# Kernel optimization log

Measured on AMD Instinct MI355X. Metric: run time of the kernel, lower is better.

## Reference

```python
import jax, jax.numpy as jnp
import numpy as np

HIDDEN = 256
RELD = 2
CAT = HIDDEN * 5 + 3  # 1283
LN_EPS = 1e-5


def setup_inputs() -> dict:
    key = jax.random.key(0)
    ks = jax.random.split(key, 13)
    b, m, h, d = 4, 256, 64, HIDDEN
    inp = {
        "point_token": jax.random.normal(ks[0], (b, m, d), jnp.float32),
        "step_hidden": jax.random.normal(ks[1], (b, h, d), jnp.float32),
        "point_dyn": jax.random.normal(ks[2], (b, m, h, d), jnp.float32),
        "point_sem": jax.random.normal(ks[3], (b, m, h, d), jnp.float32),
        "point_identity_trace": jax.random.normal(ks[4], (b, m, h, d), jnp.float32),
        "rel_pred": jax.random.normal(ks[5], (b, m, h, RELD), jnp.float32),
        "vis_prob": jax.random.uniform(ks[6], (b, m, h), jnp.float32),
        # learned params (torch Linear init scale ~ 1/sqrt(fan_in))
        "ln_gamma": jnp.ones((CAT,), jnp.float32),
        "ln_beta": jnp.zeros((CAT,), jnp.float32),
        "W1": jax.random.normal(ks[7], (CAT, d), jnp.float32) / np.sqrt(CAT),  # stored (in, out)
        "b1": jax.random.normal(ks[8], (d,), jnp.float32) / np.sqrt(CAT),
        "W2": jax.random.normal(ks[9], (d, d), jnp.float32) / np.sqrt(d),
        "b2": jax.random.normal(ks[10], (d,), jnp.float32) / np.sqrt(d),
    }
    return inp


def _forward(point_token, step_hidden, point_dyn, point_sem, point_identity_trace,
             rel_pred, vis_prob, ln_gamma, ln_beta, W1, b1, W2, b2):
    b, m, h, _ = rel_pred.shape
    x = jnp.concatenate([
        jnp.broadcast_to(point_token[:, :, None, :], (b, m, h, point_token.shape[-1])),
        jnp.broadcast_to(step_hidden[:, None, :, :], (b, m, h, step_hidden.shape[-1])),
        point_dyn,
        point_sem,
        point_identity_trace,
        rel_pred,
        vis_prob[:, :, :, None],
    ], axis=-1)  # (b, m, h, 5*d+3)
    # LayerNorm over last dim
    mu = jnp.mean(x, axis=-1, keepdims=True)
    var = jnp.mean(jnp.square(x - mu), axis=-1, keepdims=True)
    x = (x - mu) * jax.lax.rsqrt(var + LN_EPS) * ln_gamma + ln_beta
    # Linear -> GELU -> Linear -> GELU (exact erf GELU as in torch default)
    y = jax.nn.gelu(jnp.einsum('bmhc,cd->bmhd', x, W1) + b1, approximate=False)
    y = jax.nn.gelu(jnp.einsum('bmhd,de->bmhe', y, W2) + b2, approximate=False)
    return y


def reference(point_token, step_hidden, point_dyn, point_sem, point_identity_trace,
              rel_pred, vis_prob, ln_gamma, ln_beta, W1, b1, W2, b2):
    return _forward(point_token, step_hidden, point_dyn, point_sem,
                    point_identity_trace, rel_pred, vis_prob,
                    ln_gamma, ln_beta, W1, b1, W2, b2)
```

## Files before the change

### kernel.cpp

```cpp
#include <hip/hip_runtime.h>


typedef float  f32x4 __attribute__((ext_vector_type(4)));
typedef short  s16x8 __attribute__((ext_vector_type(8)));

__device__ __forceinline__ unsigned short f2bf(float f) {
    unsigned u = __builtin_bit_cast(unsigned, f);
    return (unsigned short)((u + 0x7fffu + ((u >> 16) & 1u)) >> 16);
}
__device__ __forceinline__ unsigned f2bf_pk(float lo, float hi) {
    unsigned ulo = __builtin_bit_cast(unsigned, lo);
    unsigned uhi = __builtin_bit_cast(unsigned, hi);
    ulo = (ulo + 0x7fffu + ((ulo >> 16) & 1u)) >> 16;
    uhi = (uhi + 0x7fffu + ((uhi >> 16) & 1u)) & 0xffff0000u;
    return ulo | uhi;
}
__device__ __forceinline__ float gelu_t(float x) {
    float u2 = 1.5957691216057308f * x + 0.07135481627f * (x * x * x);
    float e  = __expf(u2);
    float r  = __builtin_amdgcn_rcpf(e + 1.0f);
    return x - x * r;
}

__global__ void __launch_bounds__(256)
prep_k(const float* __restrict__ W1, const float* __restrict__ W2,
       const float* __restrict__ gamma, const float* __restrict__ beta,
       float* __restrict__ Sg, float* __restrict__ Sb,
       short* __restrict__ w1t, short* __restrict__ w2t)
{
    __shared__ float tile[32][257];
    const int blk = blockIdx.x;
    const int t   = threadIdx.x;
    const int nl  = t >> 2, c = t & 3;
    if (blk < 40) {
        float sg = 0.f, sb = 0.f;
#pragma unroll 4
        for (int kl = 0; kl < 32; ++kl) {
            int k = blk * 32 + kl;
            float w  = W1[k * 256 + t];
            float gv = gamma[k];
            tile[kl][t] = gv * w;
            sg += gv * w;
            sb += beta[k] * w;
        }
        atomicAdd(&Sg[t], sg);
        atomicAdd(&Sb[t], sb);
        __syncthreads();
#pragma unroll
        for (int gi = 0; gi < 4; ++gi) {
            int n = gi * 64 + nl;
            uint4 o;
            o.x = f2bf_pk(tile[c*8+0][n], tile[c*8+1][n]);
            o.y = f2bf_pk(tile[c*8+2][n], tile[c*8+3][n]);
            o.z = f2bf_pk(tile[c*8+4][n], tile[c*8+5][n]);
            o.w = f2bf_pk(tile[c*8+6][n], tile[c*8+7][n]);
            *(uint4*)(w1t + (blk * 256 + n) * 32 + c * 8) = o;
        }
    } else {
        const int kb = blk - 40;
#pragma unroll 4
        for (int kl = 0; kl < 32; ++kl) {
            int k = kb * 32 + kl;
            tile[kl][t] = W2[k * 256 + t];
        }
        __syncthreads();
#pragma unroll
        for (int gi = 0; gi < 4; ++gi) {
            int n = gi * 64 + nl;
            uint4 o;
            o.x = f2bf_pk(tile[c*8+0][n], tile[c*8+1][n]);
            o.y = f2bf_pk(tile[c*8+2][n], tile[c*8+3][n]);
            o.z = f2bf_pk(tile[c*8+4][n], tile[c*8+5][n]);
            o.w = f2bf_pk(tile[c*8+6][n], tile[c*8+7][n]);
            *(uint4*)(w2t + (kb * 256 + n) * 32 + c * 8) = o;
        }
    }
}

__global__ void __launch_bounds__(256, 2)
fused_main(const float* __restrict__ token, const float* __restrict__ step,
           const float* __restrict__ dyn,   const float* __restrict__ sem,
           const float* __restrict__ trace, const float* __restrict__ rel,
           const float* __restrict__ vis,   const float* __restrict__ gamma,
           const float* __restrict__ beta,  const float* __restrict__ W1,
           const float* __restrict__ b1v,   const float* __restrict__ b2v,
           const float* __restrict__ Sg,    const float* __restrict__ Sb,
           const short* __restrict__ w1t,   const short* __restrict__ w2t,
           float* __restrict__ out)
{
    __shared__ __align__(16) char lds_raw[66816];
    uint4* As                 = (uint4*)lds_raw;
    unsigned long long* As8   = (unsigned long long*)lds_raw;
    float* pst                = (float*)(lds_raw + 32768);
    float* y1f                = (float*)lds_raw;
    float* mu_s               = (float*)(lds_raw + 65536);
    float* rs_s               = mu_s + 64;
    float* t0s                = mu_s + 128;
    float* t1s                = mu_s + 192;
    float* t2s                = mu_s + 256;

    const int t    = threadIdx.x;
    const int bm   = blockIdx.x;
    const int b_i  = bm >> 8;
    const int lane = t & 63;
    const int wv   = t >> 6;
    const int l15  = lane & 15;
    const int q    = lane >> 4;
    const int n0   = wv * 64;
    const int r0   = wv * 16;

    const float* base0 = token + bm * 256;
    const float* base1 = step  + (b_i * 64 + r0) * 256;
    const float* base2 = dyn   + (bm * 64 + r0) * 256;
    const float* base3 = sem   + (bm * 64 + r0) * 256;
    const float* base4 = trace + (bm * 64 + r0) * 256;

    f32x4 acc[4][4];
    float s1[16], s2[16];
#pragma unroll
    for (int i = 0; i < 4; ++i)
#pragma unroll
        for (int j = 0; j < 4; ++j)
            acc[i][j] = (f32x4){0.f, 0.f, 0.f, 0.f};
#pragma unroll
    for (int j = 0; j < 16; ++j) { s1[j] = 0.f; s2[j] = 0.f; }

    float4 g[16];

#define LOAD_SEG(BASE, STRIDE)                                                 \
    _Pragma("unroll")                                                          \
    for (int j = 0; j < 16; ++j)                                               \
        g[j] = *((const float4*)((BASE) + j * (STRIDE)) + lane);

#define STATS_CVT_WRITE()                                                      \
    _Pragma("unroll")                                                          \
    for (int j = 0; j < 16; ++j) {                                             \
        float4 v = g[j];                                                       \
        s1[j] += v.x + v.y + v.z + v.w;                                        \
        s2[j] += v.x*v.x + v.y*v.y + v.z*v.z + v.w*v.w;                        \
        int m_ = r0 + j;                                                       \
        unsigned long long pk_ = (unsigned long long)f2bf_pk(v.x, v.y)         \
                               | ((unsigned long long)f2bf_pk(v.z, v.w) << 32);\
        As8[(m_ * 32 + ((lane >> 1) ^ (j & 7))) * 2 + (lane & 1)] = pk_;       \
    }

#define MFMA_SEG(SEG)                                                          \
    _Pragma("unroll")                                                          \
    for (int kc = 0; kc < 8; ++kc) {                                           \
        const short* wk_ = w1t + ((SEG) * 8 + kc) * 8192;                      \
        s16x8 bfr[4];                                                          \
        _Pragma("unroll")                                                      \
        for (int nt = 0; nt < 4; ++nt)                                         \
            bfr[nt] = *(const s16x8*)(wk_ + (n0 + nt * 16 + l15) * 32 + q * 8);\
        s16x8 afr[4];                                                          \
        _Pragma("unroll")                                                      \
        for (int mt = 0; mt < 4; ++mt) {                                       \
            int m_ = mt * 16 + l15;                                            \
            afr[mt] = *(const s16x8*)&As[m_ * 32 + ((kc * 4 + q) ^ (m_ & 7))]; \
        }                                                                      \
        _Pragma("unroll")                                                      \
        for (int mt = 0; mt < 4; ++mt)                                         \
            _Pragma("unroll")                                                  \
            for (int nt = 0; nt < 4; ++nt)                                     \
                acc[mt][nt] = __builtin_amdgcn_mfma_f32_16x16x32_bf16(         \
                    afr[mt], bfr[nt], acc[mt][nt], 0, 0, 0);                   \
    }

    LOAD_SEG(base0, 0);
    STATS_CVT_WRITE();
    __syncthreads();
    LOAD_SEG(base1, 256);
    MFMA_SEG(0);
    __syncthreads();
    STATS_CVT_WRITE();
    __syncthreads();
    LOAD_SEG(base2, 256);
    MFMA_SEG(1);
    __syncthreads();
    STATS_CVT_WRITE();
    __syncthreads();
    LOAD_SEG(base3, 256);
    MFMA_SEG(2);
    __syncthreads();
    STATS_CVT_WRITE();
    __syncthreads();
    LOAD_SEG(base4, 256);
    MFMA_SEG(3);
    __syncthreads();
    STATS_CVT_WRITE();
    __syncthreads();
    MFMA_SEG(4);

#pragma unroll
    for (int j = 0; j < 16; ++j) {
        int r  = r0 + j;
        int ci = (((lane >> 2) ^ (j & 7)) << 2) + (lane & 3);
        pst[r * 64 + ci]        = s1[j];
        pst[4096 + r * 64 + ci] = s2[j];
    }
    __syncthreads();

    if (t < 64) {
        const int r = t;
        float S1 = 0.f, S2 = 0.f;
#pragma unroll
        for (int i = 0; i < 16; ++i) {
            int c = i ^ (r & 7);
            const f32x4 a = *(const f32x4*)&pst[r * 64 + (c << 2)];
            const f32x4 b = *(const f32x4*)&pst[4096 + r * 64 + (c << 2)];
            S1 += a[0] + a[1] + a[2] + a[3];
            S2 += b[0] + b[1] + b[2] + b[3];
        }
        float x0 = rel[(bm * 64 + r) * 2 + 0];
        float x1 = rel[(bm * 64 + r) * 2 + 1];
        float x2 = vis[bm * 64 + r];
        S1 += x0 + x1 + x2;
        S2 += x0 * x0 + x1 * x1 + x2 * x2;
        const float inv = 1.0f / 1283.0f;
        float mu  = S1 * inv;
        float var = S2 * inv - mu * mu;
        float rs  = rsqrtf(var + 1e-5f);
        mu_s[r] = mu;
        rs_s[r] = rs;
        t0s[r] = (x0 - mu) * rs * gamma[1280] + beta[1280];
        t1s[r] = (x1 - mu) * rs * gamma[1281] + beta[1281];
        t2s[r] = (x2 - mu) * rs * gamma[1282] + beta[1282];
    }
    __syncthreads();

#pragma unroll
    for (int nt = 0; nt < 4; ++nt) {
        int n = n0 + nt * 16 + l15;
        float sg  = Sg[n], sb = Sb[n], bb = b1v[n];
        float wt0 = W1[1280 * 256 + n];
        float wt1 = W1[1281 * 256 + n];
        float wt2 = W1[1282 * 256 + n];
#pragma unroll
        for (int mt = 0; mt < 4; ++mt) {
#pragma unroll
            for (int r4 = 0; r4 < 4; ++r4) {
                int r = mt * 16 + q * 4 + r4;
                float rsv = rs_s[r], muv = mu_s[r];
                float v = rsv * acc[mt][nt][r4] - rsv * muv * sg + sb + bb
                        + t0s[r] * wt0 + t1s[r] * wt1 + t2s[r] * wt2;
                v = gelu_t(v);
                y1f[r * 256 + ((((n >> 2) ^ (r & 7)) << 2) | (n & 3))] = v;
            }
        }
    }
    __syncthreads();

    f32x4 acc2[4][4];
#pragma unroll
    for (int i = 0; i < 4; ++i)
#pragma unroll
        for (int j = 0; j < 4; ++j)
            acc2[i][j] = (f32x4){0.f, 0.f, 0.f, 0.f};

#pragma unroll
    for (int kc = 0; kc < 8; ++kc) {
        const short* wk = w2t + kc * 8192;
        s16x8 bfr[4];
#pragma unroll
        for (int nt = 0; nt < 4; ++nt)
            bfr[nt] = *(const s16x8*)(wk + (n0 + nt * 16 + l15) * 32 + q * 8);
        s16x8 afr[4];
#pragma unroll
        for (int mt = 0; mt < 4; ++mt) {
            int m  = mt * 16 + l15;
            int s  = m & 7;
            int c0 = kc * 8 + q * 2;
            const f32x4 lo = *(const f32x4*)&y1f[m * 256 + ((c0 ^ s) << 2)];
            const f32x4 hi = *(const f32x4*)&y1f[m * 256 + (((c0 + 1) ^ s) << 2)];
            unsigned p0, p1, p2, p3;
            asm("v_cvt_pk_bf16_f32 %0, %1, %2" : "=v"(p0) : "v"(lo[0]), "v"(lo[1]));
            asm("v_cvt_pk_bf16_f32 %0, %1, %2" : "=v"(p1) : "v"(lo[2]), "v"(lo[3]));
            asm("v_cvt_pk_bf16_f32 %0, %1, %2" : "=v"(p2) : "v"(hi[0]), "v"(hi[1]));
            asm("v_cvt_pk_bf16_f32 %0, %1, %2" : "=v"(p3) : "v"(hi[2]), "v"(hi[3]));
            uint4 u;
            u.x = p0; u.y = p1; u.z = p2; u.w = p3;
            afr[mt] = __builtin_bit_cast(s16x8, u);
        }
#pragma unroll
        for (int mt = 0; mt < 4; ++mt)
#pragma unroll
            for (int nt = 0; nt < 4; ++nt)
                acc2[mt][nt] = __builtin_amdgcn_mfma_f32_16x16x32_bf16(
                    afr[mt], bfr[nt], acc2[mt][nt], 0, 0, 0);
    }

#pragma unroll
    for (int nt = 0; nt < 4; ++nt) {
        int n = n0 + nt * 16 + l15;
        float bb = b2v[n];
#pragma unroll
        for (int mt = 0; mt < 4; ++mt)
#pragma unroll
            for (int r4 = 0; r4 < 4; ++r4) {
                int r = mt * 16 + q * 4 + r4;
                out[(bm * 64 + r) * 256 + n] = gelu_t(acc2[mt][nt][r4] + bb);
            }
    }
#undef LOAD_SEG
#undef STATS_CVT_WRITE
#undef MFMA_SEG
}

extern "C" void kernel_launch(void* const* d_in, const int* in_sizes, int n_in,
                              void* d_out, int out_size, void* d_ws, size_t ws_size,
                              hipStream_t stream) {
    const float* token = (const float*)d_in[0];
    const float* step  = (const float*)d_in[1];
    const float* dyn   = (const float*)d_in[2];
    const float* sem   = (const float*)d_in[3];
    const float* trace = (const float*)d_in[4];
    const float* rel   = (const float*)d_in[5];
    const float* vis   = (const float*)d_in[6];
    const float* gamma = (const float*)d_in[7];
    const float* beta  = (const float*)d_in[8];
    const float* W1    = (const float*)d_in[9];
    const float* b1    = (const float*)d_in[10];
    const float* W2    = (const float*)d_in[11];
    const float* b2    = (const float*)d_in[12];

    float* Sg  = (float*)d_ws;
    float* Sb  = Sg + 256;
    short* w1t = (short*)((char*)d_ws + 2048);
    short* w2t = w1t + 1280 * 256;
    float* out = (float*)d_out;

    hipMemsetAsync(d_ws, 0, 2048, stream);
    hipLaunchKernelGGL(prep_k, dim3(48), dim3(256), 0, stream,
                       W1, W2, gamma, beta, Sg, Sb, w1t, w2t);
    hipLaunchKernelGGL(fused_main, dim3(1024), dim3(256), 0, stream,
                       token, step, dyn, sem, trace, rel, vis, gamma, beta,
                       W1, b1, b2, Sg, Sb, w1t, w2t, out);
}
```

Baseline: 306.5 us.

## Double-buffer LDS segments with 8 waves and shuffle-based LayerNorm stats

The main kernel moves from 4 to 8 waves per block, each wave owning 8 rows for loading and 32 output columns for the GEMMs. It ping-pongs between two LDS buffers so the bf16 pack and global loads of the next segment overlap the MFMA work on the current one, and it raises MFMA issue priority with s_setprio. Row statistics are now reduced with wave shuffles instead of an LDS staging pass. The prep kernel computes the gamma/beta column sums in a dedicated block, which removes the memset and the atomics. In exchange, each wave does less MFMA work per A-fragment load, and launch_bounds(512,4) with about 66KB of LDS per block may not reach the occupancy it asks for.

```diff
diff --git a/kernel.cpp b/kernel.cpp
--- a/kernel.cpp
+++ b/kernel.cpp
@@ -33,18 +33,11 @@
     const int t   = threadIdx.x;
     const int nl  = t >> 2, c = t & 3;
     if (blk < 40) {
-        float sg = 0.f, sb = 0.f;
 #pragma unroll 4
         for (int kl = 0; kl < 32; ++kl) {
             int k = blk * 32 + kl;
-            float w  = W1[k * 256 + t];
-            float gv = gamma[k];
-            tile[kl][t] = gv * w;
-            sg += gv * w;
-            sb += beta[k] * w;
-        }
-        atomicAdd(&Sg[t], sg);
-        atomicAdd(&Sb[t], sb);
+            tile[kl][t] = gamma[k] * W1[k * 256 + t];
+        }
         __syncthreads();
 #pragma unroll
         for (int gi = 0; gi < 4; ++gi) {
@@ -56,7 +49,7 @@
             o.w = f2bf_pk(tile[c*8+6][n], tile[c*8+7][n]);
             *(uint4*)(w1t + (blk * 256 + n) * 32 + c * 8) = o;
         }
-    } else {
+    } else if (blk < 48) {
         const int kb = blk - 40;
 #pragma unroll 4
         for (int kl = 0; kl < 32; ++kl) {
@@ -74,10 +67,21 @@
             o.w = f2bf_pk(tile[c*8+6][n], tile[c*8+7][n]);
             *(uint4*)(w2t + (kb * 256 + n) * 32 + c * 8) = o;
         }
-    }
-}
-
-__global__ void __launch_bounds__(256, 2)
+    } else {
+        const int n = t;
+        float sg = 0.f, sb = 0.f;
+#pragma unroll 8
+        for (int k = 0; k < 1280; ++k) {
+            float w = W1[k * 256 + n];
+            sg += gamma[k] * w;
+            sb += beta[k]  * w;
+        }
+        Sg[n] = sg;
+        Sb[n] = sb;
+    }
+}
+
+__global__ void __launch_bounds__(512, 4)
 fused_main(const float* __restrict__ token, const float* __restrict__ step,
            const float* __restrict__ dyn,   const float* __restrict__ sem,
            const float* __restrict__ trace, const float* __restrict__ rel,
@@ -89,9 +93,10 @@
            float* __restrict__ out)
 {
     __shared__ __align__(16) char lds_raw[66816];
-    uint4* As                 = (uint4*)lds_raw;
-    unsigned long long* As8   = (unsigned long long*)lds_raw;
-    float* pst                = (float*)(lds_raw + 32768);
+    uint4* bufA               = (uint4*)lds_raw;
+    uint4* bufB               = (uint4*)(lds_raw + 32768);
+    unsigned long long* bufA8 = (unsigned long long*)lds_raw;
+    unsigned long long* bufB8 = (unsigned long long*)(lds_raw + 32768);
     float* y1f                = (float*)lds_raw;
     float* mu_s               = (float*)(lds_raw + 65536);
     float* rs_s               = mu_s + 64;
@@ -106,8 +111,9 @@
     const int wv   = t >> 6;
     const int l15  = lane & 15;
     const int q    = lane >> 4;
-    const int n0   = wv * 64;
-    const int r0   = wv * 16;
+    const int sw   = l15 & 7;
+    const int n0   = wv * 32;
+    const int r0   = wv * 8;
 
     const float* base0 = token + bm * 256;
     const float* base1 = step  + (b_i * 64 + r0) * 256;
@@ -115,121 +121,126 @@
     const float* base3 = sem   + (bm * 64 + r0) * 256;
     const float* base4 = trace + (bm * 64 + r0) * 256;
 
-    f32x4 acc[4][4];
-    float s1[16], s2[16];
+    f32x4 acc[2][2];
+    float s1[8], s2[8];
+    float4 g[8];
+    unsigned long long pk[8];
+#pragma unroll
+    for (int i = 0; i < 2; ++i)
+#pragma unroll
+        for (int j = 0; j < 2; ++j)
+            acc[i][j] = (f32x4){0.f, 0.f, 0.f, 0.f};
+    f32x4 acc4[4][2];
 #pragma unroll
     for (int i = 0; i < 4; ++i)
 #pragma unroll
-        for (int j = 0; j < 4; ++j)
-            acc[i][j] = (f32x4){0.f, 0.f, 0.f, 0.f};
-#pragma unroll
-    for (int j = 0; j < 16; ++j) { s1[j] = 0.f; s2[j] = 0.f; }
-
-    float4 g[16];
-
-#define LOAD_SEG(BASE, STRIDE)                                                 \
+        for (int j = 0; j < 2; ++j)
+            acc4[i][j] = (f32x4){0.f, 0.f, 0.f, 0.f};
+#pragma unroll
+    for (int j = 0; j < 8; ++j) { s1[j] = 0.f; s2[j] = 0.f; }
+
+#define LOADSEG(BASE, STRIDE)                                                  \
     _Pragma("unroll")                                                          \
-    for (int j = 0; j < 16; ++j)                                               \
+    for (int j = 0; j < 8; ++j)                                                \
         g[j] = *((const float4*)((BASE) + j * (STRIDE)) + lane);
 
-#define STATS_CVT_WRITE()                                                      \
+#define PACKSEG()                                                              \
     _Pragma("unroll")                                                          \
-    for (int j = 0; j < 16; ++j) {                                             \
+    for (int j = 0; j < 8; ++j) {                                              \
         float4 v = g[j];                                                       \
         s1[j] += v.x + v.y + v.z + v.w;                                        \
         s2[j] += v.x*v.x + v.y*v.y + v.z*v.z + v.w*v.w;                        \
-        int m_ = r0 + j;                                                       \
-        unsigned long long pk_ = (unsigned long long)f2bf_pk(v.x, v.y)         \
-                               | ((unsigned long long)f2bf_pk(v.z, v.w) << 32);\
-        As8[(m_ * 32 + ((lane >> 1) ^ (j & 7))) * 2 + (lane & 1)] = pk_;       \
-    }
-
-#define MFMA_SEG(SEG)                                                          \
+        pk[j] = (unsigned long long)f2bf_pk(v.x, v.y)                          \
+              | ((unsigned long long)f2bf_pk(v.z, v.w) << 32);                 \
+    }
+
+#define WRITESEG(BUF8)                                                         \
     _Pragma("unroll")                                                          \
-    for (int kc = 0; kc < 8; ++kc) {                                           \
-        const short* wk_ = w1t + ((SEG) * 8 + kc) * 8192;                      \
-        s16x8 bfr[4];                                                          \
-        _Pragma("unroll")                                                      \
-        for (int nt = 0; nt < 4; ++nt)                                         \
-            bfr[nt] = *(const s16x8*)(wk_ + (n0 + nt * 16 + l15) * 32 + q * 8);\
-        s16x8 afr[4];                                                          \
-        _Pragma("unroll")                                                      \
-        for (int mt = 0; mt < 4; ++mt) {                                       \
-            int m_ = mt * 16 + l15;                                            \
-            afr[mt] = *(const s16x8*)&As[m_ * 32 + ((kc * 4 + q) ^ (m_ & 7))]; \
-        }                                                                      \
-        _Pragma("unroll")                                                      \
-        for (int mt = 0; mt < 4; ++mt)                                         \
-            _Pragma("unroll")                                                  \
-            for (int nt = 0; nt < 4; ++nt)                                     \
-                acc[mt][nt] = __builtin_amdgcn_mfma_f32_16x16x32_bf16(         \
-                    afr[mt], bfr[nt], acc[mt][nt], 0, 0, 0);                   \
-    }
-
-    LOAD_SEG(base0, 0);
-    STATS_CVT_WRITE();
-    __syncthreads();
-    LOAD_SEG(base1, 256);
-    MFMA_SEG(0);
-    __syncthreads();
-    STATS_CVT_WRITE();
-    __syncthreads();
-    LOAD_SEG(base2, 256);
-    MFMA_SEG(1);
-    __syncthreads();
-    STATS_CVT_WRITE();
-    __syncthreads();
-    LOAD_SEG(base3, 256);
-    MFMA_SEG(2);
-    __syncthreads();
-    STATS_CVT_WRITE();
-    __syncthreads();
-    LOAD_SEG(base4, 256);
-    MFMA_SEG(3);
-    __syncthreads();
-    STATS_CVT_WRITE();
-    __syncthreads();
-    MFMA_SEG(4);
-
-#pragma unroll
-    for (int j = 0; j < 16; ++j) {
-        int r  = r0 + j;
-        int ci = (((lane >> 2) ^ (j & 7)) << 2) + (lane & 3);
-        pst[r * 64 + ci]        = s1[j];
-        pst[4096 + r * 64 + ci] = s2[j];
-    }
-    __syncthreads();
-
-    if (t < 64) {
-        const int r = t;
-        float S1 = 0.f, S2 = 0.f;
-#pragma unroll
-        for (int i = 0; i < 16; ++i) {
-            int c = i ^ (r & 7);
-            const f32x4 a = *(const f32x4*)&pst[r * 64 + (c << 2)];
-            const f32x4 b = *(const f32x4*)&pst[4096 + r * 64 + (c << 2)];
-            S1 += a[0] + a[1] + a[2] + a[3];
-            S2 += b[0] + b[1] + b[2] + b[3];
-        }
-        float x0 = rel[(bm * 64 + r) * 2 + 0];
-        float x1 = rel[(bm * 64 + r) * 2 + 1];
-        float x2 = vis[bm * 64 + r];
-        S1 += x0 + x1 + x2;
-        S2 += x0 * x0 + x1 * x1 + x2 * x2;
-        const float inv = 1.0f / 1283.0f;
-        float mu  = S1 * inv;
-        float var = S2 * inv - mu * mu;
-        float rs  = rsqrtf(var + 1e-5f);
-        mu_s[r] = mu;
-        rs_s[r] = rs;
-        t0s[r] = (x0 - mu) * rs * gamma[1280] + beta[1280];
-        t1s[r] = (x1 - mu) * rs * gamma[1281] + beta[1281];
-        t2s[r] = (x2 - mu) * rs * gamma[1282] + beta[1282];
-    }
-    __syncthreads();
-
-#pragma unroll
-    for (int nt = 0; nt < 4; ++nt) {
+    for (int j = 0; j < 8; ++j)                                                \
+        (BUF8)[((r0 + j) * 32 + ((lane >> 1) ^ j)) * 2 + (lane & 1)] = pk[j];
+
+#define G1_KC(SEG, KC, BUF)                                                    \
+    do {                                                                       \
+        const short* wk_ = w1t + ((SEG) * 8 + (KC)) * 8192;                    \
+        s16x8 b0 = *(const s16x8*)(wk_ + (n0 + l15) * 32 + q * 8);             \
+        s16x8 b1 = *(const s16x8*)(wk_ + (n0 + 16 + l15) * 32 + q * 8);        \
+        s16x8 a0 = *(const s16x8*)&(BUF)[( 0 + l15) * 32 + (((KC)*4+q) ^ sw)]; \
+        s16x8 a1 = *(const s16x8*)&(BUF)[(16 + l15) * 32 + (((KC)*4+q) ^ sw)]; \
+        __builtin_amdgcn_s_setprio(1);                                         \
+        acc4[0][0] = __builtin_amdgcn_mfma_f32_16x16x32_bf16(a0, b0, acc4[0][0], 0,0,0); \
+        acc4[0][1] = __builtin_amdgcn_mfma_f32_16x16x32_bf16(a0, b1, acc4[0][1], 0,0,0); \
+        acc4[1][0] = __builtin_amdgcn_mfma_f32_16x16x32_bf16(a1, b0, acc4[1][0], 0,0,0); \
+        acc4[1][1] = __builtin_amdgcn_mfma_f32_16x16x32_bf16(a1, b1, acc4[1][1], 0,0,0); \
+        __builtin_amdgcn_s_setprio(0);                                         \
+        s16x8 a2 = *(const s16x8*)&(BUF)[(32 + l15) * 32 + (((KC)*4+q) ^ sw)]; \
+        s16x8 a3 = *(const s16x8*)&(BUF)[(48 + l15) * 32 + (((KC)*4+q) ^ sw)]; \
+        __builtin_amdgcn_s_setprio(1);                                         \
+        acc4[2][0] = __builtin_amdgcn_mfma_f32_16x16x32_bf16(a2, b0, acc4[2][0], 0,0,0); \
+        acc4[2][1] = __builtin_amdgcn_mfma_f32_16x16x32_bf16(a2, b1, acc4[2][1], 0,0,0); \
+        acc4[3][0] = __builtin_amdgcn_mfma_f32_16x16x32_bf16(a3, b0, acc4[3][0], 0,0,0); \
+        acc4[3][1] = __builtin_amdgcn_mfma_f32_16x16x32_bf16(a3, b1, acc4[3][1], 0,0,0); \
+        __builtin_amdgcn_s_setprio(0);                                         \
+    } while (0)
+
+#define G1_HALF1(SEG, BUF) do { G1_KC(SEG,0,BUF); G1_KC(SEG,1,BUF); G1_KC(SEG,2,BUF); G1_KC(SEG,3,BUF); } while (0)
+#define G1_HALF2(SEG, BUF) do { G1_KC(SEG,4,BUF); G1_KC(SEG,5,BUF); G1_KC(SEG,6,BUF); G1_KC(SEG,7,BUF); } while (0)
+
+    LOADSEG(base0, 0);      PACKSEG();  WRITESEG(bufA8);
+    LOADSEG(base1, 256);    PACKSEG();  WRITESEG(bufB8);
+    LOADSEG(base2, 256);
+    __syncthreads();
+
+    G1_HALF1(0, bufA);  PACKSEG();  LOADSEG(base3, 256);  G1_HALF2(0, bufA);
+    __syncthreads();
+    WRITESEG(bufA8);
+    G1_HALF1(1, bufB);  PACKSEG();  LOADSEG(base4, 256);  G1_HALF2(1, bufB);
+    __syncthreads();
+    WRITESEG(bufB8);
+    G1_HALF1(2, bufA);  PACKSEG();                        G1_HALF2(2, bufA);
+    __syncthreads();
+    WRITESEG(bufA8);
+    G1_HALF1(3, bufB);  G1_HALF2(3, bufB);
+    __syncthreads();
+    G1_HALF1(4, bufA);  G1_HALF2(4, bufA);
+
+#pragma unroll
+    for (int j = 0; j < 8; ++j) {
+#pragma unroll
+        for (int d = 1; d < 64; d <<= 1) {
+            s1[j] += __shfl_xor(s1[j], d);
+            s2[j] += __shfl_xor(s2[j], d);
+        }
+    }
+    {
+        float S1v = s1[0], S2v = s2[0];
+        const int rsel = lane & 7;
+#pragma unroll
+        for (int j = 1; j < 8; ++j) {
+            bool p = (rsel == j);
+            S1v = p ? s1[j] : S1v;
+            S2v = p ? s2[j] : S2v;
+        }
+        if (lane < 8) {
+            const int r = r0 + rsel;
+            float2 rl = *(const float2*)(rel + (bm * 64 + r) * 2);
+            float x2  = vis[bm * 64 + r];
+            float S1 = S1v + rl.x + rl.y + x2;
+            float S2 = S2v + rl.x * rl.x + rl.y * rl.y + x2 * x2;
+            const float inv = 1.0f / 1283.0f;
+            float mu  = S1 * inv;
+            float var = S2 * inv - mu * mu;
+            float rs  = rsqrtf(var + 1e-5f);
+            mu_s[r] = mu;
+            rs_s[r] = rs;
+            t0s[r] = (rl.x - mu) * rs * gamma[1280] + beta[1280];
+            t1s[r] = (rl.y - mu) * rs * gamma[1281] + beta[1281];
+            t2s[r] = (x2   - mu) * rs * gamma[1282] + beta[1282];
+        }
+    }
+    __syncthreads();
+
+#pragma unroll
+    for (int nt = 0; nt < 2; ++nt) {
         int n = n0 + nt * 16 + l15;
         float sg  = Sg[n], sb = Sb[n], bb = b1v[n];
         float wt0 = W1[1280 * 256 + n];
@@ -241,7 +252,7 @@
             for (int r4 = 0; r4 < 4; ++r4) {
                 int r = mt * 16 + q * 4 + r4;
                 float rsv = rs_s[r], muv = mu_s[r];
-                float v = rsv * acc[mt][nt][r4] - rsv * muv * sg + sb + bb
+                float v = rsv * acc4[mt][nt][r4] - rsv * muv * sg + sb + bb
                         + t0s[r] * wt0 + t1s[r] * wt1 + t2s[r] * wt2;
                 v = gelu_t(v);
                 y1f[r * 256 + ((((n >> 2) ^ (r & 7)) << 2) | (n & 3))] = v;
@@ -250,20 +261,18 @@
     }
     __syncthreads();
 
-    f32x4 acc2[4][4];
+    f32x4 acc2[4][2];
 #pragma unroll
     for (int i = 0; i < 4; ++i)
 #pragma unroll
-        for (int j = 0; j < 4; ++j)
+        for (int j = 0; j < 2; ++j)
             acc2[i][j] = (f32x4){0.f, 0.f, 0.f, 0.f};
 
 #pragma unroll
     for (int kc = 0; kc < 8; ++kc) {
         const short* wk = w2t + kc * 8192;
-        s16x8 bfr[4];
-#pragma unroll
-        for (int nt = 0; nt < 4; ++nt)
-            bfr[nt] = *(const s16x8*)(wk + (n0 + nt * 16 + l15) * 32 + q * 8);
+        s16x8 b0 = *(const s16x8*)(wk + (n0 + l15) * 32 + q * 8);
+        s16x8 b1 = *(const s16x8*)(wk + (n0 + 16 + l15) * 32 + q * 8);
         s16x8 afr[4];
 #pragma unroll
         for (int mt = 0; mt < 4; ++mt) {
@@ -281,16 +290,17 @@
             u.x = p0; u.y = p1; u.z = p2; u.w = p3;
             afr[mt] = __builtin_bit_cast(s16x8, u);
         }
-#pragma unroll
-        for (int mt = 0; mt < 4; ++mt)
-#pragma unroll
-            for (int nt = 0; nt < 4; ++nt)
-                acc2[mt][nt] = __builtin_amdgcn_mfma_f32_16x16x32_bf16(
-                    afr[mt], bfr[nt], acc2[mt][nt], 0, 0, 0);
-    }
-
-#pragma unroll
-    for (int nt = 0; nt < 4; ++nt) {
+        __builtin_amdgcn_s_setprio(1);
+#pragma unroll
+        for (int mt = 0; mt < 4; ++mt) {
+            acc2[mt][0] = __builtin_amdgcn_mfma_f32_16x16x32_bf16(afr[mt], b0, acc2[mt][0], 0,0,0);
+            acc2[mt][1] = __builtin_amdgcn_mfma_f32_16x16x32_bf16(afr[mt], b1, acc2[mt][1], 0,0,0);
+        }
+        __builtin_amdgcn_s_setprio(0);
+    }
+
+#pragma unroll
+    for (int nt = 0; nt < 2; ++nt) {
         int n = n0 + nt * 16 + l15;
         float bb = b2v[n];
 #pragma unroll
@@ -301,9 +311,12 @@
                 out[(bm * 64 + r) * 256 + n] = gelu_t(acc2[mt][nt][r4] + bb);
             }
     }
-#undef LOAD_SEG
-#undef STATS_CVT_WRITE
-#undef MFMA_SEG
+#undef LOADSEG
+#undef PACKSEG
+#undef WRITESEG
+#undef G1_KC
+#undef G1_HALF1
+#undef G1_HALF2
 }
 
 extern "C" void kernel_launch(void* const* d_in, const int* in_sizes, int n_in,
@@ -329,10 +342,9 @@
     short* w2t = w1t + 1280 * 256;
     float* out = (float*)d_out;
 
-    hipMemsetAsync(d_ws, 0, 2048, stream);
-    hipLaunchKernelGGL(prep_k, dim3(48), dim3(256), 0, stream,
+    hipLaunchKernelGGL(prep_k, dim3(49), dim3(256), 0, stream,
                        W1, W2, gamma, beta, Sg, Sb, w1t, w2t);
-    hipLaunchKernelGGL(fused_main, dim3(1024), dim3(256), 0, stream,
+    hipLaunchKernelGGL(fused_main, dim3(1024), dim3(512), 0, stream,
                        token, step, dyn, sem, trace, rel, vis, gamma, beta,
                        W1, b1, b2, Sg, Sb, w1t, w2t, out);
 }
```

Measured after the change: 557.4 us. +81.9%, slower.

## Halve LDS footprint by storing GELU output as bf16 and raising occupancy

Applied to the files above, without the earlier changes.

The first-layer GELU output is now written to LDS as bf16 in a swizzled layout that matches the A-operand buffer, so the second GEMM reads MFMA fragments directly with no per-load conversion. Together with aliasing the stats scratch onto the same region, this cuts LDS from about 66KB to about 34KB, and launch bounds are raised to 4 blocks per CU. Separately, the Sg/Sb column sums move out of atomics into a dedicated 49th prep block, which removes the memset. The risk is register pressure under the higher launch bound, and a single slow serial block in prep that loops over 1280 rows.

```diff
diff --git a/kernel.cpp b/kernel.cpp
--- a/kernel.cpp
+++ b/kernel.cpp
@@ -33,18 +33,11 @@
     const int t   = threadIdx.x;
     const int nl  = t >> 2, c = t & 3;
     if (blk < 40) {
-        float sg = 0.f, sb = 0.f;
 #pragma unroll 4
         for (int kl = 0; kl < 32; ++kl) {
             int k = blk * 32 + kl;
-            float w  = W1[k * 256 + t];
-            float gv = gamma[k];
-            tile[kl][t] = gv * w;
-            sg += gv * w;
-            sb += beta[k] * w;
-        }
-        atomicAdd(&Sg[t], sg);
-        atomicAdd(&Sb[t], sb);
+            tile[kl][t] = gamma[k] * W1[k * 256 + t];
+        }
         __syncthreads();
 #pragma unroll
         for (int gi = 0; gi < 4; ++gi) {
@@ -56,7 +49,7 @@
             o.w = f2bf_pk(tile[c*8+6][n], tile[c*8+7][n]);
             *(uint4*)(w1t + (blk * 256 + n) * 32 + c * 8) = o;
         }
-    } else {
+    } else if (blk < 48) {
         const int kb = blk - 40;
 #pragma unroll 4
         for (int kl = 0; kl < 32; ++kl) {
@@ -74,10 +67,21 @@
             o.w = f2bf_pk(tile[c*8+6][n], tile[c*8+7][n]);
             *(uint4*)(w2t + (kb * 256 + n) * 32 + c * 8) = o;
         }
-    }
-}
-
-__global__ void __launch_bounds__(256, 2)
+    } else {
+        const int n = t;
+        float sg = 0.f, sb = 0.f;
+#pragma unroll 8
+        for (int k = 0; k < 1280; ++k) {
+            float w = W1[k * 256 + n];
+            sg += gamma[k] * w;
+            sb += beta[k]  * w;
+        }
+        Sg[n] = sg;
+        Sb[n] = sb;
+    }
+}
+
+__global__ void __launch_bounds__(256, 4)
 fused_main(const float* __restrict__ token, const float* __restrict__ step,
            const float* __restrict__ dyn,   const float* __restrict__ sem,
            const float* __restrict__ trace, const float* __restrict__ rel,
@@ -88,12 +92,12 @@
            const short* __restrict__ w1t,   const short* __restrict__ w2t,
            float* __restrict__ out)
 {
-    __shared__ __align__(16) char lds_raw[66816];
+    __shared__ __align__(16) char lds_raw[34048];
     uint4* As                 = (uint4*)lds_raw;
     unsigned long long* As8   = (unsigned long long*)lds_raw;
-    float* pst                = (float*)(lds_raw + 32768);
-    float* y1f                = (float*)lds_raw;
-    float* mu_s               = (float*)(lds_raw + 65536);
+    float* pst                = (float*)lds_raw;
+    unsigned short* y16       = (unsigned short*)lds_raw;
+    float* mu_s               = (float*)(lds_raw + 32768);
     float* rs_s               = mu_s + 64;
     float* t0s                = mu_s + 128;
     float* t1s                = mu_s + 192;
@@ -190,6 +194,7 @@
     STATS_CVT_WRITE();
     __syncthreads();
     MFMA_SEG(4);
+    __syncthreads();
 
 #pragma unroll
     for (int j = 0; j < 16; ++j) {
@@ -244,7 +249,8 @@
                 float v = rsv * acc[mt][nt][r4] - rsv * muv * sg + sb + bb
                         + t0s[r] * wt0 + t1s[r] * wt1 + t2s[r] * wt2;
                 v = gelu_t(v);
-                y1f[r * 256 + ((((n >> 2) ^ (r & 7)) << 2) | (n & 3))] = v;
+                int chunk = (n >> 3) ^ (r & 7);
+                y16[(r * 32 + chunk) * 8 + (n & 7)] = f2bf(v);
             }
         }
     }
@@ -267,19 +273,8 @@
         s16x8 afr[4];
 #pragma unroll
         for (int mt = 0; mt < 4; ++mt) {
-            int m  = mt * 16 + l15;
-            int s  = m & 7;
-            int c0 = kc * 8 + q * 2;
-            const f32x4 lo = *(const f32x4*)&y1f[m * 256 + ((c0 ^ s) << 2)];
-            const f32x4 hi = *(const f32x4*)&y1f[m * 256 + (((c0 + 1) ^ s) << 2)];
-            unsigned p0, p1, p2, p3;
-            asm("v_cvt_pk_bf16_f32 %0, %1, %2" : "=v"(p0) : "v"(lo[0]), "v"(lo[1]));
-            asm("v_cvt_pk_bf16_f32 %0, %1, %2" : "=v"(p1) : "v"(lo[2]), "v"(lo[3]));
-            asm("v_cvt_pk_bf16_f32 %0, %1, %2" : "=v"(p2) : "v"(hi[0]), "v"(hi[1]));
-            asm("v_cvt_pk_bf16_f32 %0, %1, %2" : "=v"(p3) : "v"(hi[2]), "v"(hi[3]));
-            uint4 u;
-            u.x = p0; u.y = p1; u.z = p2; u.w = p3;
-            afr[mt] = __builtin_bit_cast(s16x8, u);
+            int m_ = mt * 16 + l15;
+            afr[mt] = *(const s16x8*)&As[m_ * 32 + ((kc * 4 + q) ^ (m_ & 7))];
         }
 #pragma unroll
         for (int mt = 0; mt < 4; ++mt)
@@ -329,8 +324,7 @@
     short* w2t = w1t + 1280 * 256;
     float* out = (float*)d_out;
 
-    hipMemsetAsync(d_ws, 0, 2048, stream);
-    hipLaunchKernelGGL(prep_k, dim3(48), dim3(256), 0, stream,
+    hipLaunchKernelGGL(prep_k, dim3(49), dim3(256), 0, stream,
                        W1, W2, gamma, beta, Sg, Sb, w1t, w2t);
     hipLaunchKernelGGL(fused_main, dim3(1024), dim3(256), 0, stream,
                        token, step, dyn, sem, trace, rel, vis, gamma, beta,
```

Result: slower. 584.7 us (+90.8%).
